# Performance work log

Measured on AMD Instinct MI355X. Metric: run time of the kernel, lower is better.

## Reference

```python
import jax, jax.numpy as jnp
import numpy as np

BN_EPS = 1e-5

@jax.custom_vjp
def bsign(x):
    # forward: sign(x) (torch semantics: sign(0)=0, matched by jnp.sign)
    return jnp.sign(x)

def _bsign_fwd(x):
    return jnp.sign(x), x

def _bsign_bwd(x, g):
    # straight-through estimator: pass grad where |x| <= 1, zero elsewhere
    return (g * (jnp.abs(x) <= 1.0).astype(g.dtype),)

bsign.defvjp(_bsign_fwd, _bsign_bwd)


def setup_inputs() -> dict:
    key = jax.random.key(0)
    k1, k2 = jax.random.split(key, 2)
    B, IN, OUT = 8192, 2048, 2048
    x = jax.random.normal(k1, (B, IN), dtype=jnp.float32)
    weight = jax.random.normal(k2, (OUT, IN), dtype=jnp.float32) * 0.1
    gamma = jnp.ones((OUT,), dtype=jnp.float32)
    beta = jnp.zeros((OUT,), dtype=jnp.float32)
    return {"x": x, "weight": weight, "gamma": gamma, "beta": beta}


def reference(x, weight, gamma, beta):
    # binarize input and weight to {-1, 0, +1} via sign (STE in bwd)
    xb = bsign(x)            # [B, IN]
    wb = bsign(weight)       # [OUT, IN]
    out = xb @ wb.T          # [B, OUT] full-precision GEMM over +/-1 values
    # BatchNorm1d, training mode: normalize with biased batch statistics
    mean = jnp.mean(out, axis=0)                 # [OUT]
    var = jnp.var(out, axis=0)                   # biased (ddof=0), matches torch BN
    out = (out - mean) * jax.lax.rsqrt(var + BN_EPS) * gamma + beta
    return out
```

## Files before the change

kernel.cpp:

```cpp
#include <hip/hip_runtime.h>
#include <stdint.h>


typedef int int32x4 __attribute__((ext_vector_type(4)));

#define BM 128
#define BN 128
#define BKI 128
#define EPS_BN 1e-5f

__device__ __forceinline__ void load16_lds(const void* g, void* l) {
  __builtin_amdgcn_global_load_lds(
      (const __attribute__((address_space(1))) void*)g,
      (__attribute__((address_space(3))) void*)l,
      16, 0, 0);
}

__device__ __forceinline__ char sgn(float v) {
  return v > 0.f ? (char)1 : (v < 0.f ? (char)-1 : (char)0);
}

__global__ void binarize_kernel(const float* __restrict__ x,
                                const float* __restrict__ w,
                                char* __restrict__ Ab, char* __restrict__ Bb,
                                float* __restrict__ stats,
                                int nx4, int ntot4, int n2) {
  int idx = blockIdx.x * blockDim.x + threadIdx.x;
  if (idx < n2) stats[idx] = 0.f;
  if (idx >= ntot4) return;
  const float4* src;
  char* dst;
  int i;
  if (idx < nx4) {
    src = reinterpret_cast<const float4*>(x); dst = Ab; i = idx;
  } else {
    src = reinterpret_cast<const float4*>(w); dst = Bb; i = idx - nx4;
  }
  float4 v = src[i];
  char4 o;
  o.x = sgn(v.x); o.y = sgn(v.y); o.z = sgn(v.z); o.w = sgn(v.w);
  reinterpret_cast<char4*>(dst)[i] = o;
}

__global__ __launch_bounds__(256, 4) void gemm_i8_kernel(
    const char* __restrict__ A,
    const char* __restrict__ Bt,
    short* __restrict__ Craw,
    float* __restrict__ colSum,
    float* __restrict__ colSq,
    int M, int N, int K) {
  __shared__ __align__(16) char sA[BM * BKI];
  __shared__ __align__(16) char sB[BN * BKI];

  const int tid  = threadIdx.x;
  const int wave = tid >> 6;
  const int lane = tid & 63;

  const int nby = M / BM;
  const int rowBlock = (blockIdx.x % nby) * BM;
  const int colBlock = (blockIdx.x / nby) * BN;

  const int laneRow = lane >> 3;
  const int c       = lane & 7;
  const int swz     = ((c ^ laneRow) & 7) * 16;

  const char* Ag = A  + (size_t)(rowBlock + wave * 32 + laneRow) * K + swz;
  const char* Bg = Bt + (size_t)(colBlock + wave * 32 + laneRow) * K + swz;
  char* sAw = &sA[(wave * 32) * BKI];
  char* sBw = &sB[(wave * 32) * BKI];

  const int f    = lane & 15;
  const int quad = lane >> 4;
  const int wr = (wave >> 1) * 64;
  const int wc = (wave & 1) * 64;
  const int f7 = f & 7;

  int32x4 acc[4][4] = {};

  for (int k0 = 0; k0 < K; k0 += BKI) {
    __syncthreads();
#pragma unroll
    for (int i = 0; i < 4; ++i) {
      load16_lds(Ag + k0 + (size_t)(i * 8) * K, sAw + i * 8 * BKI);
      load16_lds(Bg + k0 + (size_t)(i * 8) * K, sBw + i * 8 * BKI);
    }
    __syncthreads();

#pragma unroll
    for (int s = 0; s < 2; ++s) {
      const int chunk = ((s * 4 + quad) ^ f7) * 16;
      int32x4 af[4], bfr[4];
#pragma unroll
      for (int mi = 0; mi < 4; ++mi)
        af[mi] = *reinterpret_cast<const int32x4*>(
            &sA[(wr + mi * 16 + f) * BKI + chunk]);
#pragma unroll
      for (int ni = 0; ni < 4; ++ni)
        bfr[ni] = *reinterpret_cast<const int32x4*>(
            &sB[(wc + ni * 16 + f) * BKI + chunk]);
#pragma unroll
      for (int mi = 0; mi < 4; ++mi)
#pragma unroll
        for (int ni = 0; ni < 4; ++ni)
          acc[mi][ni] = __builtin_amdgcn_mfma_i32_16x16x64_i8(
              af[mi], bfr[ni], acc[mi][ni], 0, 0, 0);
    }
  }

#pragma unroll
  for (int ni = 0; ni < 4; ++ni) {
    const int col = colBlock + wc + ni * 16 + f;
    float s = 0.f, sq = 0.f;
#pragma unroll
    for (int mi = 0; mi < 4; ++mi) {
      short* Cp = Craw + (size_t)(rowBlock + wr + mi * 16 + quad * 4) * N + col;
#pragma unroll
      for (int r = 0; r < 4; ++r) {
        const int v = acc[mi][ni][r];
        Cp[(size_t)r * N] = (short)v;
        const float fv = (float)v;
        s += fv;
        sq += fv * fv;
      }
    }
    s  += __shfl_xor(s, 16);  s  += __shfl_xor(s, 32);
    sq += __shfl_xor(sq, 16); sq += __shfl_xor(sq, 32);
    if (quad == 0) {
      atomicAdd(&colSum[col], s);
      atomicAdd(&colSq[col], sq);
    }
  }
}

__global__ void norm_kernel(const short* __restrict__ Craw,
                            float* __restrict__ C,
                            const float* __restrict__ colSum,
                            const float* __restrict__ colSq,
                            const float* __restrict__ gamma,
                            const float* __restrict__ beta,
                            int ncol4mask, int ncol4shift, int halfRows,
                            float invM) {
  const int idx = blockIdx.x * blockDim.x + threadIdx.x;
  const int c4  = idx & ncol4mask;
  const int row = idx >> ncol4shift;
  const int col = c4 * 4;
  const int ncol4 = ncol4mask + 1;

  const float4 sm = *reinterpret_cast<const float4*>(&colSum[col]);
  const float4 sv = *reinterpret_cast<const float4*>(&colSq[col]);
  const float4 g  = *reinterpret_cast<const float4*>(&gamma[col]);
  const float4 b  = *reinterpret_cast<const float4*>(&beta[col]);

  float4 sc, sh;
  {
    float m, vv;
    m = sm.x * invM; vv = sv.x * invM - m * m;
    sc.x = g.x * rsqrtf(vv + EPS_BN); sh.x = b.x - m * sc.x;
    m = sm.y * invM; vv = sv.y * invM - m * m;
    sc.y = g.y * rsqrtf(vv + EPS_BN); sh.y = b.y - m * sc.y;
    m = sm.z * invM; vv = sv.z * invM - m * m;
    sc.z = g.z * rsqrtf(vv + EPS_BN); sh.z = b.z - m * sc.z;
    m = sm.w * invM; vv = sv.w * invM - m * m;
    sc.w = g.w * rsqrtf(vv + EPS_BN); sh.w = b.w - m * sc.w;
  }

#pragma unroll
  for (int h = 0; h < 2; ++h) {
    const size_t e = (size_t)(row + h * halfRows) * ncol4 + c4;
    const short4 rv = reinterpret_cast<const short4*>(Craw)[e];
    float4 o;
    o.x = (float)rv.x * sc.x + sh.x;
    o.y = (float)rv.y * sc.y + sh.y;
    o.z = (float)rv.z * sc.z + sh.z;
    o.w = (float)rv.w * sc.w + sh.w;
    reinterpret_cast<float4*>(C)[e] = o;
  }
}

extern "C" void kernel_launch(void* const* d_in, const int* in_sizes, int n_in,
                              void* d_out, int out_size, void* d_ws,
                              size_t ws_size, hipStream_t stream) {
  const float* x     = (const float*)d_in[0];
  const float* w     = (const float*)d_in[1];
  const float* gamma = (const float*)d_in[2];
  const float* beta  = (const float*)d_in[3];
  float* C = (float*)d_out;

  const int N = in_sizes[2];
  const int K = in_sizes[1] / N;
  const int M = in_sizes[0] / K;

  char* ws = (char*)d_ws;
  char* Abin = ws;
  char* Bbin = ws + (size_t)M * K;
  short* Craw = (short*)(ws + (size_t)M * K + (size_t)N * K);
  float* stats = (float*)((char*)Craw + (size_t)M * N * sizeof(short));
  float* colSum = stats;
  float* colSq  = stats + N;

  {
    int nx4 = (M * K) / 4;
    int ntot4 = (M * K + N * K) / 4;
    binarize_kernel<<<(ntot4 + 255) / 256, 256, 0, stream>>>(
        x, w, Abin, Bbin, stats, nx4, ntot4, 2 * N);
  }

  const int nTiles = (M / BM) * (N / BN);
  gemm_i8_kernel<<<nTiles, 256, 0, stream>>>(Abin, Bbin, Craw, colSum, colSq,
                                             M, N, K);

  {
    int ncol4 = N / 4;
    int shift = 0;
    while ((1 << shift) < ncol4) ++shift;
    int total = (M / 2) * ncol4;
    norm_kernel<<<(total + 255) / 256, 256, 0, stream>>>(
        Craw, C, colSum, colSq, gamma, beta, ncol4 - 1, shift, M / 2,
        1.0f / (float)M);
  }
}
```

Baseline: 179.5 us.

## Double-buffer LDS tiles in int8 GEMM with halved K-step

Replaces the single-buffered 128-wide K tile with two 64-wide LDS buffers. Each iteration prefetches the next tile via global_load_lds while the current tile is read and fed to MFMAs, and needs only one barrier per iteration instead of two. The swizzle is adapted to 4 chunks per row. This halves the MFMA work per iteration, and correct ordering relies on the barrier waiting for the outstanding async LDS loads.

Result: slower. 186.1 us (+3.6%).

```diff
diff --git a/kernel.cpp b/kernel.cpp
--- a/kernel.cpp
+++ b/kernel.cpp
@@ -6,7 +6,7 @@
 
 #define BM 128
 #define BN 128
-#define BKI 128
+#define BKI 64
 #define EPS_BN 1e-5f
 
 __device__ __forceinline__ void load16_lds(const void* g, void* l) {
@@ -49,8 +49,7 @@
     float* __restrict__ colSum,
     float* __restrict__ colSq,
     int M, int N, int K) {
-  __shared__ __align__(16) char sA[BM * BKI];
-  __shared__ __align__(16) char sB[BN * BKI];
+  __shared__ __align__(16) char sT[2][BM * BKI + BN * BKI];
 
   const int tid  = threadIdx.x;
   const int wave = tid >> 6;
@@ -60,51 +59,62 @@
   const int rowBlock = (blockIdx.x % nby) * BM;
   const int colBlock = (blockIdx.x / nby) * BN;
 
-  const int laneRow = lane >> 3;
-  const int c       = lane & 7;
-  const int swz     = ((c ^ laneRow) & 7) * 16;
+  const int laneRow = lane >> 2;
+  const int c       = lane & 3;
+  const int swz     = ((c ^ laneRow) & 3) * 16;
 
   const char* Ag = A  + (size_t)(rowBlock + wave * 32 + laneRow) * K + swz;
   const char* Bg = Bt + (size_t)(colBlock + wave * 32 + laneRow) * K + swz;
-  char* sAw = &sA[(wave * 32) * BKI];
-  char* sBw = &sB[(wave * 32) * BKI];
+  const int sAoff = (wave * 32) * BKI;
+  const int sBoff = BM * BKI + (wave * 32) * BKI;
 
   const int f    = lane & 15;
   const int quad = lane >> 4;
   const int wr = (wave >> 1) * 64;
   const int wc = (wave & 1) * 64;
-  const int f7 = f & 7;
+  const int rchunk = quad ^ (f & 3);
 
   int32x4 acc[4][4] = {};
 
+#pragma unroll
+  for (int i = 0; i < 2; ++i) {
+    load16_lds(Ag + (size_t)(i * 16) * K, &sT[0][sAoff + i * 16 * BKI]);
+    load16_lds(Bg + (size_t)(i * 16) * K, &sT[0][sBoff + i * 16 * BKI]);
+  }
+
+  int p = 0;
   for (int k0 = 0; k0 < K; k0 += BKI) {
     __syncthreads();
-#pragma unroll
-    for (int i = 0; i < 4; ++i) {
-      load16_lds(Ag + k0 + (size_t)(i * 8) * K, sAw + i * 8 * BKI);
-      load16_lds(Bg + k0 + (size_t)(i * 8) * K, sBw + i * 8 * BKI);
+
+    int32x4 af[4], bfr[4];
+#pragma unroll
+    for (int mi = 0; mi < 4; ++mi)
+      af[mi] = *reinterpret_cast<const int32x4*>(
+          &sT[p][(wr + mi * 16 + f) * BKI + rchunk * 16]);
+#pragma unroll
+    for (int ni = 0; ni < 4; ++ni)
+      bfr[ni] = *reinterpret_cast<const int32x4*>(
+          &sT[p][BM * BKI + (wc + ni * 16 + f) * BKI + rchunk * 16]);
+
+    const int kn = k0 + BKI;
+    if (kn < K) {
+#pragma unroll
+      for (int i = 0; i < 2; ++i) {
+        load16_lds(Ag + kn + (size_t)(i * 16) * K,
+                   &sT[p ^ 1][sAoff + i * 16 * BKI]);
+        load16_lds(Bg + kn + (size_t)(i * 16) * K,
+                   &sT[p ^ 1][sBoff + i * 16 * BKI]);
+      }
     }
-    __syncthreads();
-
-#pragma unroll
-    for (int s = 0; s < 2; ++s) {
-      const int chunk = ((s * 4 + quad) ^ f7) * 16;
-      int32x4 af[4], bfr[4];
-#pragma unroll
-      for (int mi = 0; mi < 4; ++mi)
-        af[mi] = *reinterpret_cast<const int32x4*>(
-            &sA[(wr + mi * 16 + f) * BKI + chunk]);
+
+#pragma unroll
+    for (int mi = 0; mi < 4; ++mi)
 #pragma unroll
       for (int ni = 0; ni < 4; ++ni)
-        bfr[ni] = *reinterpret_cast<const int32x4*>(
-            &sB[(wc + ni * 16 + f) * BKI + chunk]);
-#pragma unroll
-      for (int mi = 0; mi < 4; ++mi)
-#pragma unroll
-        for (int ni = 0; ni < 4; ++ni)
-          acc[mi][ni] = __builtin_amdgcn_mfma_i32_16x16x64_i8(
-              af[mi], bfr[ni], acc[mi][ni], 0, 0, 0);
-    }
+        acc[mi][ni] = __builtin_amdgcn_mfma_i32_16x16x64_i8(
+            af[mi], bfr[ni], acc[mi][ni], 0, 0, 0);
+
+    p ^= 1;
   }
 
 #pragma unroll
```

## Fuse binarize, GEMM and batchnorm into one cooperative kernel with grid syncs

Applied to the files above, without the earlier changes.

Replaces the three-kernel pipeline with one cooperatively launched kernel. It binarizes inputs with a grid-stride loop, syncs the grid, runs the int8 MFMA GEMM, accumulates column statistics with atomics, syncs again, then normalizes straight from the accumulator registers. This drops the int16 intermediate write and re-read and two kernel launches. The cost is two grid-wide barriers, and it relies on all 1024 tiles being co-resident. If the cooperative launch fails, it falls back to the old three-kernel path.

Result: slower. 394.1 us (+119.5%).

```diff
diff --git a/kernel.cpp b/kernel.cpp
--- a/kernel.cpp
+++ b/kernel.cpp
@@ -1,5 +1,8 @@
 #include <hip/hip_runtime.h>
+#include <hip/hip_cooperative_groups.h>
 #include <stdint.h>
+
+namespace cg = cooperative_groups;
 
 
 typedef int int32x4 __attribute__((ext_vector_type(4)));
@@ -20,11 +23,151 @@
   return v > 0.f ? (char)1 : (v < 0.f ? (char)-1 : (char)0);
 }
 
+__device__ __forceinline__ void gemm_core(
+    const char* __restrict__ A, const char* __restrict__ Bt,
+    int rowBlock, int colBlock, int K, char* sA, char* sB,
+    int wave, int lane, int32x4 acc[4][4]) {
+  const int laneRow = lane >> 3;
+  const int c       = lane & 7;
+  const int swz     = ((c ^ laneRow) & 7) * 16;
+
+  const char* Ag = A  + (size_t)(rowBlock + wave * 32 + laneRow) * K + swz;
+  const char* Bg = Bt + (size_t)(colBlock + wave * 32 + laneRow) * K + swz;
+  char* sAw = &sA[(wave * 32) * BKI];
+  char* sBw = &sB[(wave * 32) * BKI];
+
+  const int f    = lane & 15;
+  const int quad = lane >> 4;
+  const int wr = (wave >> 1) * 64;
+  const int wc = (wave & 1) * 64;
+  const int f7 = f & 7;
+
+  for (int k0 = 0; k0 < K; k0 += BKI) {
+    __syncthreads();
+#pragma unroll
+    for (int i = 0; i < 4; ++i) {
+      load16_lds(Ag + k0 + (size_t)(i * 8) * K, sAw + i * 8 * BKI);
+      load16_lds(Bg + k0 + (size_t)(i * 8) * K, sBw + i * 8 * BKI);
+    }
+    __syncthreads();
+
+#pragma unroll
+    for (int s = 0; s < 2; ++s) {
+      const int chunk = ((s * 4 + quad) ^ f7) * 16;
+      int32x4 af[4], bfr[4];
+#pragma unroll
+      for (int mi = 0; mi < 4; ++mi)
+        af[mi] = *reinterpret_cast<const int32x4*>(
+            &sA[(wr + mi * 16 + f) * BKI + chunk]);
+#pragma unroll
+      for (int ni = 0; ni < 4; ++ni)
+        bfr[ni] = *reinterpret_cast<const int32x4*>(
+            &sB[(wc + ni * 16 + f) * BKI + chunk]);
+#pragma unroll
+      for (int mi = 0; mi < 4; ++mi)
+#pragma unroll
+        for (int ni = 0; ni < 4; ++ni)
+          acc[mi][ni] = __builtin_amdgcn_mfma_i32_16x16x64_i8(
+              af[mi], bfr[ni], acc[mi][ni], 0, 0, 0);
+    }
+  }
+}
+
+__global__ __launch_bounds__(256, 4) void bnn_fused_kernel(
+    const float* __restrict__ x, const float* __restrict__ w,
+    const float* __restrict__ gamma, const float* __restrict__ beta,
+    char* __restrict__ Abin, char* __restrict__ Bbin,
+    float* __restrict__ colSum, float* __restrict__ colSq,
+    float* __restrict__ C, int M, int N, int K) {
+  cg::grid_group grid = cg::this_grid();
+
+  const int tid  = threadIdx.x;
+  const int gtid = blockIdx.x * blockDim.x + tid;
+  const int gstride = gridDim.x * blockDim.x;
+
+  if (gtid < 2 * N) colSum[gtid] = 0.f;
+  {
+    const int nx4 = (M * K) / 4;
+    const int ntot = nx4 + (N * K) / 4;
+    for (int idx = gtid; idx < ntot; idx += gstride) {
+      const float4* src;
+      char* dst;
+      int i;
+      if (idx < nx4) {
+        src = reinterpret_cast<const float4*>(x); dst = Abin; i = idx;
+      } else {
+        src = reinterpret_cast<const float4*>(w); dst = Bbin; i = idx - nx4;
+      }
+      float4 v = src[i];
+      char4 o;
+      o.x = sgn(v.x); o.y = sgn(v.y); o.z = sgn(v.z); o.w = sgn(v.w);
+      reinterpret_cast<char4*>(dst)[i] = o;
+    }
+  }
+
+  grid.sync();
+
+  __shared__ __align__(16) char sA[BM * BKI];
+  __shared__ __align__(16) char sB[BN * BKI];
+
+  const int wave = tid >> 6;
+  const int lane = tid & 63;
+  const int nby = M / BM;
+  const int rowBlock = (blockIdx.x % nby) * BM;
+  const int colBlock = (blockIdx.x / nby) * BN;
+
+  int32x4 acc[4][4] = {};
+  gemm_core(Abin, Bbin, rowBlock, colBlock, K, sA, sB, wave, lane, acc);
+
+  const int f    = lane & 15;
+  const int quad = lane >> 4;
+  const int wr = (wave >> 1) * 64;
+  const int wc = (wave & 1) * 64;
+#pragma unroll
+  for (int ni = 0; ni < 4; ++ni) {
+    const int col = colBlock + wc + ni * 16 + f;
+    float s = 0.f, sq = 0.f;
+#pragma unroll
+    for (int mi = 0; mi < 4; ++mi)
+#pragma unroll
+      for (int r = 0; r < 4; ++r) {
+        const float fv = (float)acc[mi][ni][r];
+        s += fv;
+        sq += fv * fv;
+      }
+    s  += __shfl_xor(s, 16);  s  += __shfl_xor(s, 32);
+    sq += __shfl_xor(sq, 16); sq += __shfl_xor(sq, 32);
+    if (quad == 0) {
+      atomicAdd(&colSum[col], s);
+      atomicAdd(&colSq[col], sq);
+    }
+  }
+
+  grid.sync();
+
+  const float invM = 1.0f / (float)M;
+#pragma unroll
+  for (int ni = 0; ni < 4; ++ni) {
+    const int col = colBlock + wc + ni * 16 + f;
+    const float mean = colSum[col] * invM;
+    const float var  = colSq[col] * invM - mean * mean;
+    const float sc   = gamma[col] * rsqrtf(var + EPS_BN);
+    const float sh   = beta[col] - mean * sc;
+#pragma unroll
+    for (int mi = 0; mi < 4; ++mi) {
+      float* Cp = C + (size_t)(rowBlock + wr + mi * 16 + quad * 4) * N + col;
+#pragma unroll
+      for (int r = 0; r < 4; ++r)
+        Cp[(size_t)r * N] = (float)acc[mi][ni][r] * sc + sh;
+    }
+  }
+}
+
 __global__ void binarize_kernel(const float* __restrict__ x,
                                 const float* __restrict__ w,
                                 char* __restrict__ Ab, char* __restrict__ Bb,
-                                float* __restrict__ stats,
-                                int nx4, int ntot4, int n2) {
+                                float* __restrict__ stats, int nx4, int ntot4,
+                                int n2) {
   int idx = blockIdx.x * blockDim.x + threadIdx.x;
   if (idx < n2) stats[idx] = 0.f;
   if (idx >= ntot4) return;
@@ -43,70 +186,22 @@
 }
 
 __global__ __launch_bounds__(256, 4) void gemm_i8_kernel(
-    const char* __restrict__ A,
-    const char* __restrict__ Bt,
-    short* __restrict__ Craw,
-    float* __restrict__ colSum,
-    float* __restrict__ colSq,
-    int M, int N, int K) {
+    const char* __restrict__ A, const char* __restrict__ Bt,
+    short* __restrict__ Craw, float* __restrict__ colSum,
+    float* __restrict__ colSq, int M, int N, int K) {
   __shared__ __align__(16) char sA[BM * BKI];
   __shared__ __align__(16) char sB[BN * BKI];
-
-  const int tid  = threadIdx.x;
-  const int wave = tid >> 6;
-  const int lane = tid & 63;
-
+  const int tid = threadIdx.x;
+  const int wave = tid >> 6, lane = tid & 63;
   const int nby = M / BM;
   const int rowBlock = (blockIdx.x % nby) * BM;
   const int colBlock = (blockIdx.x / nby) * BN;
 
-  const int laneRow = lane >> 3;
-  const int c       = lane & 7;
-  const int swz     = ((c ^ laneRow) & 7) * 16;
-
-  const char* Ag = A  + (size_t)(rowBlock + wave * 32 + laneRow) * K + swz;
-  const char* Bg = Bt + (size_t)(colBlock + wave * 32 + laneRow) * K + swz;
-  char* sAw = &sA[(wave * 32) * BKI];
-  char* sBw = &sB[(wave * 32) * BKI];
-
-  const int f    = lane & 15;
-  const int quad = lane >> 4;
-  const int wr = (wave >> 1) * 64;
-  const int wc = (wave & 1) * 64;
-  const int f7 = f & 7;
-
   int32x4 acc[4][4] = {};
-
-  for (int k0 = 0; k0 < K; k0 += BKI) {
-    __syncthreads();
-#pragma unroll
-    for (int i = 0; i < 4; ++i) {
-      load16_lds(Ag + k0 + (size_t)(i * 8) * K, sAw + i * 8 * BKI);
-      load16_lds(Bg + k0 + (size_t)(i * 8) * K, sBw + i * 8 * BKI);
-    }
-    __syncthreads();
-
-#pragma unroll
-    for (int s = 0; s < 2; ++s) {
-      const int chunk = ((s * 4 + quad) ^ f7) * 16;
-      int32x4 af[4], bfr[4];
-#pragma unroll
-      for (int mi = 0; mi < 4; ++mi)
-        af[mi] = *reinterpret_cast<const int32x4*>(
-            &sA[(wr + mi * 16 + f) * BKI + chunk]);
-#pragma unroll
-      for (int ni = 0; ni < 4; ++ni)
-        bfr[ni] = *reinterpret_cast<const int32x4*>(
-            &sB[(wc + ni * 16 + f) * BKI + chunk]);
-#pragma unroll
-      for (int mi = 0; mi < 4; ++mi)
-#pragma unroll
-        for (int ni = 0; ni < 4; ++ni)
-          acc[mi][ni] = __builtin_amdgcn_mfma_i32_16x16x64_i8(
-              af[mi], bfr[ni], acc[mi][ni], 0, 0, 0);
-    }
-  }
-
+  gemm_core(A, Bt, rowBlock, colBlock, K, sA, sB, wave, lane, acc);
+
+  const int f = lane & 15, quad = lane >> 4;
+  const int wr = (wave >> 1) * 64, wc = (wave & 1) * 64;
 #pragma unroll
   for (int ni = 0; ni < 4; ++ni) {
     const int col = colBlock + wc + ni * 16 + f;
@@ -137,9 +232,8 @@
                             const float* __restrict__ colSum,
                             const float* __restrict__ colSq,
                             const float* __restrict__ gamma,
-                            const float* __restrict__ beta,
-                            int ncol4mask, int ncol4shift, int halfRows,
-                            float invM) {
+                            const float* __restrict__ beta, int ncol4mask,
+                            int ncol4shift, int halfRows, float invM) {
   const int idx = blockIdx.x * blockDim.x + threadIdx.x;
   const int c4  = idx & ncol4mask;
   const int row = idx >> ncol4shift;
@@ -186,9 +280,9 @@
   const float* beta  = (const float*)d_in[3];
   float* C = (float*)d_out;
 
-  const int N = in_sizes[2];
-  const int K = in_sizes[1] / N;
-  const int M = in_sizes[0] / K;
+  int N = in_sizes[2];
+  int K = in_sizes[1] / N;
+  int M = in_sizes[0] / K;
 
   char* ws = (char*)d_ws;
   char* Abin = ws;
@@ -198,18 +292,21 @@
   float* colSum = stats;
   float* colSq  = stats + N;
 
-  {
+  const int nTiles = (M / BM) * (N / BN);
+
+  void* args[] = {&x, &w, &gamma, &beta, &Abin, &Bbin,
+                  &colSum, &colSq, &C, &M, &N, &K};
+  hipError_t err = hipLaunchCooperativeKernel(
+      (const void*)bnn_fused_kernel, dim3(nTiles), dim3(256), args, 0, stream);
+
+  if (err != hipSuccess) {
+    (void)hipGetLastError();
     int nx4 = (M * K) / 4;
     int ntot4 = (M * K + N * K) / 4;
     binarize_kernel<<<(ntot4 + 255) / 256, 256, 0, stream>>>(
         x, w, Abin, Bbin, stats, nx4, ntot4, 2 * N);
-  }
-
-  const int nTiles = (M / BM) * (N / BN);
-  gemm_i8_kernel<<<nTiles, 256, 0, stream>>>(Abin, Bbin, Craw, colSum, colSq,
-                                             M, N, K);
-
-  {
+    gemm_i8_kernel<<<nTiles, 256, 0, stream>>>(Abin, Bbin, Craw, colSum, colSq,
+                                               M, N, K);
     int ncol4 = N / 4;
     int shift = 0;
     while ((1 << shift) < ncol4) ++shift;
```
